# Kernel optimization log

Hardware: AMD Instinct MI355X
Metric: run time of the kernel (lower is better)

## Reference

```python
import jax, jax.numpy as jnp
import numpy as np
from jax import lax

B, S = 16, 512
H = 512          # hidden_size == embedding_dim (required by the module's own wiring)
V = 10000        # dict_len
G = 4 * H


def setup_inputs() -> dict:
    key = jax.random.key(0)
    ks = jax.random.split(key, 16)
    sc = 0.05
    inp = {
        "source": jax.random.randint(ks[0], (B, S), 0, V),
        "w_emb": jax.random.normal(ks[1], (H, V), jnp.float32) * sc,
        "b_emb": jax.random.normal(ks[2], (H,), jnp.float32) * sc,
        "w_ih0": jax.random.normal(ks[3], (G, H), jnp.float32) * sc,
        "w_hh0": jax.random.normal(ks[4], (G, H), jnp.float32) * sc,
        "b_ih0": jax.random.normal(ks[5], (G,), jnp.float32) * sc,
        "b_hh0": jax.random.normal(ks[6], (G,), jnp.float32) * sc,
        "w_ih1": jax.random.normal(ks[7], (G, H), jnp.float32) * sc,
        "w_hh1": jax.random.normal(ks[8], (G, H), jnp.float32) * sc,
        "b_ih1": jax.random.normal(ks[9], (G,), jnp.float32) * sc,
        "b_hh1": jax.random.normal(ks[10], (G,), jnp.float32) * sc,
        "w1": jax.random.normal(ks[11], (128, H), jnp.float32) * sc,
        "b1": jax.random.normal(ks[12], (128,), jnp.float32) * sc,
        "w2": jax.random.normal(ks[13], (V, 128), jnp.float32) * sc,
        "b2": jax.random.normal(ks[14], (V,), jnp.float32) * sc,
    }
    return inp


def _lstm_layer(x, w_ih, w_hh, b_ih, b_hh):
    # x: [B, S, H] -> hs: [B, S, H]; PyTorch gate order i, f, g, o
    b, s, _ = x.shape
    h_dim = w_hh.shape[1]
    # precompute input projections for all timesteps
    x_proj = jnp.einsum('bsd,gd->bsg', x, w_ih) + b_ih + b_hh  # [B, S, 4H]

    def step(carry, xt):
        h, c = carry
        gates = xt + h @ w_hh.T                      # [B, 4H]
        i, f, g, o = jnp.split(gates, 4, axis=-1)
        i = jax.nn.sigmoid(i)
        f = jax.nn.sigmoid(f)
        g = jnp.tanh(g)
        o = jax.nn.sigmoid(o)
        c = f * c + i * g
        h = o * jnp.tanh(c)
        return (h, c), h

    h0 = jnp.zeros((b, h_dim), x.dtype)
    c0 = jnp.zeros((b, h_dim), x.dtype)
    _, hs = lax.scan(step, (h0, c0), jnp.swapaxes(x_proj, 0, 1))  # [S, B, H]
    return jnp.swapaxes(hs, 0, 1)


def reference(source, w_emb, b_emb,
              w_ih0, w_hh0, b_ih0, b_hh0,
              w_ih1, w_hh1, b_ih1, b_hh1,
              w1, b1, w2, b2):
    # one_hot(source) @ w_emb.T + b_emb == row-gather of w_emb.T (identical math)
    emb = jnp.take(w_emb.T, source, axis=0) + b_emb        # [B, S, H]
    h = _lstm_layer(emb, w_ih0, w_hh0, b_ih0, b_hh0)
    h = _lstm_layer(h, w_ih1, w_hh1, b_ih1, b_hh1)         # dropout identity at eval
    hid = jax.nn.relu(jnp.einsum('bsh,kh->bsk', h, w1) + b1)  # [B, S, 128]
    logits = jnp.einsum('bsk,vk->bsv', hid, w2) + b2       # [B, S, V]
    return logits
```

## Files before the change

kernel.cpp:

```cpp
#include <hip/hip_runtime.h>
#include <hip/hip_bf16.h>

#define B_ 16
#define S_ 512
#define H_ 512
#define V_ 10000
#define G_ 2048
#define M_ (B_*S_)

typedef short bf16x8 __attribute__((ext_vector_type(8)));
typedef float f32x4 __attribute__((ext_vector_type(4)));
typedef _Float16 f16x8 __attribute__((ext_vector_type(8)));

static __device__ __forceinline__ unsigned short f2bf(float x) {
    union { float f; unsigned int u; } v; v.f = x;
    unsigned int r = v.u + 0x7fffu + ((v.u >> 16) & 1u);
    return (unsigned short)(r >> 16);
}
static __device__ __forceinline__ unsigned short f2h_bits(float x) {
    _Float16 h = (_Float16)x;
    return __builtin_bit_cast(unsigned short, h);
}
static __device__ __forceinline__ float ftanh(float x) {
    float ax = fabsf(x);
    float e  = __expf(-2.f*ax);
    float r  = (1.f - e) / (1.f + e);
    return copysignf(r, x);
}

__global__ void prep_kernel(const float* __restrict__ w_ih0, const float* __restrict__ w_hh0,
                            const float* __restrict__ b_ih0, const float* __restrict__ b_hh0,
                            const float* __restrict__ w_ih1, const float* __restrict__ w_hh1,
                            const float* __restrict__ b_ih1, const float* __restrict__ b_hh1,
                            const float* __restrict__ w1,   const float* __restrict__ w2,
                            unsigned short* __restrict__ w_ih0_b, _Float16* __restrict__ wfrag0,
                            _Float16* __restrict__ wfrag1x,      _Float16* __restrict__ wfrag1h,
                            unsigned short* __restrict__ w1_b,    unsigned short* __restrict__ w2_b,
                            float* __restrict__ bias0, float* __restrict__ bias1,
                            unsigned int* __restrict__ l1prog, unsigned int* __restrict__ lc_slot) {
    if (blockIdx.x == 0 && threadIdx.x == 0) atomicAdd(lc_slot, 1u);
    if (blockIdx.x == 0 && threadIdx.x < 64) l1prog[threadIdx.x*16] = 0u;
    int i  = blockIdx.x * blockDim.x + threadIdx.x;
    int st = gridDim.x * blockDim.x;
    for (int k = i; k < G_*H_; k += st) w_ih0_b[k] = f2bf(w_ih0[k]);
    for (int d = i; d < G_*H_; d += st) {
        int e    = d & 7;
        int l    = (d >> 3) & 63;
        int wrow = (d >> 9) & 7;
        int kc   = (d >> 12) & 15;
        int j    = (d >> 16) & 15;
        int r    = wrow*16 + (l & 15);
        int R    = (r >> 5)*512 + j*32 + (r & 31);
        int k    = kc*32 + ((l >> 4) << 3) + e;
        wfrag0[d] = (_Float16)w_hh0[R*H_ + k];
    }
    for (int d = i; d < G_*H_; d += st) {
        int e    = d & 7;
        int l    = (d >> 3) & 63;
        int nt   = (d >> 9) & 1;
        int kc   = (d >> 10) & 15;
        int j    = (d >> 14) & 63;
        int r    = nt*16 + (l & 15);
        int R    = (r >> 3)*512 + j*8 + (r & 7);
        int k    = kc*32 + ((l >> 4) << 3) + e;
        wfrag1x[d] = (_Float16)w_ih1[R*H_ + k];
        wfrag1h[d] = (_Float16)w_hh1[R*H_ + k];
    }
    for (int k = i; k < V_*128; k += st) w2_b[k] = f2bf(w2[k]);
    for (int k = i; k < 128*H_; k += st) w1_b[k] = f2bf(w1[k]);
    for (int k = i; k < G_;     k += st) { bias0[k] = b_ih0[k] + b_hh0[k]; bias1[k] = b_ih1[k] + b_hh1[k]; }
}

__global__ void embed_kernel(const int* __restrict__ src, const float* __restrict__ w_emb,
                             const float* __restrict__ b_emb, unsigned short* __restrict__ emb) {
    int m = blockIdx.x;
    int idx = src[m];
    for (int h = threadIdx.x; h < H_; h += blockDim.x)
        emb[(long)m*H_ + h] = f2bf(w_emb[(long)h*V_ + idx] + b_emb[h]);
}

template<bool RELU, bool OUT_BF16>
__launch_bounds__(256)
__global__ void gemm_kernel(const unsigned short* __restrict__ A, const unsigned short* __restrict__ Bm,
                            const float* __restrict__ bias, void* __restrict__ Cout,
                            int Ndim, int K) {
    __shared__ unsigned short At[128*40];
    __shared__ unsigned short Bt[128*40];
    int m0 = blockIdx.y * 128;
    int n0 = blockIdx.x * 128;
    int tid  = threadIdx.x;
    int lane = tid & 63, wave = tid >> 6;
    int wm = (wave >> 1) * 64, wn = (wave & 1) * 64;
    int l15 = lane & 15, l4 = lane >> 4;
    f32x4 acc[4][4] = {};

    for (int kk = 0; kk < K; kk += 32) {
        __syncthreads();
        #pragma unroll
        for (int rep = 0; rep < 2; ++rep) {
            int gid = tid + rep*256;
            int row = gid >> 2, c8 = (gid & 3) << 3;
            *(uint4*)&At[row*40 + c8] = *(const uint4*)&A[(long)(m0+row)*K + kk + c8];
            int nrow = n0 + row; if (nrow >= Ndim) nrow = Ndim - 1;
            *(uint4*)&Bt[row*40 + c8] = *(const uint4*)&Bm[(long)nrow*K + kk + c8];
        }
        __syncthreads();
        bf16x8 af[4], bfr[4];
        #pragma unroll
        for (int i = 0; i < 4; ++i)
            af[i] = *(const bf16x8*)&At[(wm + i*16 + l15)*40 + l4*8];
        #pragma unroll
        for (int j = 0; j < 4; ++j)
            bfr[j] = *(const bf16x8*)&Bt[(wn + j*16 + l15)*40 + l4*8];
        #pragma unroll
        for (int i = 0; i < 4; ++i)
            #pragma unroll
            for (int j = 0; j < 4; ++j)
                acc[i][j] = __builtin_amdgcn_mfma_f32_16x16x32_bf16(af[i], bfr[j], acc[i][j], 0, 0, 0);
    }

    #pragma unroll
    for (int i = 0; i < 4; ++i) {
        int row = m0 + wm + i*16 + l4*4;
        #pragma unroll
        for (int j = 0; j < 4; ++j) {
            int col = n0 + wn + j*16 + l15;
            if (col < Ndim) {
                float bv = bias[col];
                #pragma unroll
                for (int r = 0; r < 4; ++r) {
                    float v = acc[i][j][r] + bv;
                    if (RELU) v = v > 0.f ? v : 0.f;
                    if (OUT_BF16) ((unsigned short*)Cout)[(long)(row+r)*Ndim + col] = f2bf(v);
                    else          ((float*)Cout)[(long)(row+r)*Ndim + col] = v;
                }
            }
        }
    }
}

__launch_bounds__(512)
__global__ void lstm_fused_kernel(const float* __restrict__ xp,
                                  const uint4* __restrict__ wfrag0,
                                  const uint4* __restrict__ wfrag1x,
                                  const uint4* __restrict__ wfrag1h,
                                  const float* __restrict__ bias1,
                                  unsigned long long* __restrict__ h0ex,
                                  unsigned long long* __restrict__ h1ex,
                                  unsigned int* __restrict__ l1prog,
                                  const unsigned int* __restrict__ lc_slot,
                                  unsigned short* __restrict__ hout) {
    __shared__ __align__(16) char smem[156160];
    int tid  = threadIdx.x;
    int lane = tid & 63, wave = tid >> 6;
    int l15  = lane & 15, l4 = lane >> 4;
    unsigned int base = __hip_atomic_load(lc_slot, __ATOMIC_RELAXED, __HIP_MEMORY_SCOPE_AGENT) << 16;

    if (blockIdx.x < 16) {
        uint4*     w_lds = (uint4*)smem;
        _Float16*  h_lds = (_Float16*)(smem + 131072);
        float*     gbuf  = (float*)(smem + 131072 + 16640);
        int j = blockIdx.x;
        for (int i = tid; i < 8192; i += 512) w_lds[i] = wfrag0[(long)j*8192 + i];
        for (int i = tid; i < 4160; i += 512) ((unsigned int*)h_lds)[i] = 0;
        __syncthreads();
        const _Float16* wh = (const _Float16*)w_lds;
        int ch = tid >> 5, s = tid & 31;
        float c = 0.f;

        for (int t = 0; t < S_; ++t) {
            const float* xr = xp + ((long)ch*S_ + t)*G_ + j*32 + s;
            float xi = xr[0], xf = xr[512], xg = xr[1024], xo = xr[1536];
            if (wave == 0 && t >= 16 && (t & 7) == 0) {
                unsigned int thr = base + (unsigned int)(t - 8);
                unsigned int pv = __hip_atomic_load(l1prog + lane*16, __ATOMIC_RELAXED, __HIP_MEMORY_SCOPE_AGENT);
                while (!__all((int)(pv >= thr))) {
                    __builtin_amdgcn_s_sleep(4);
                    pv = __hip_atomic_load(l1prog + lane*16, __ATOMIC_RELAXED, __HIP_MEMORY_SCOPE_AGENT);
                }
            }
            if (t > 0) {
                unsigned int tagv = base + (unsigned int)t;
                const unsigned long long* bse = h0ex + (long)((t-1) & 15)*4096;
                unsigned long long v[8];
                for (;;) {
                    #pragma unroll
                    for (int q = 0; q < 8; ++q)
                        v[q] = __hip_atomic_load(bse + q*512 + tid, __ATOMIC_RELAXED, __HIP_MEMORY_SCOPE_AGENT);
                    bool ok = true;
                    #pragma unroll
                    for (int q = 0; q < 8; ++q)
                        ok &= ((unsigned int)(v[q] >> 32) == tagv);
                    if (ok) break;
                    __builtin_amdgcn_s_sleep(1);
                }
                #pragma unroll
                for (int q = 0; q < 8; ++q) {
                    int w = q*512 + tid;
                    *(unsigned int*)&h_lds[(w >> 8)*520 + (w & 255)*2] = (unsigned int)v[q];
                }
            }
            __syncthreads();
            f32x4 acc = {0.f,0.f,0.f,0.f};
            #pragma unroll
            for (int kc = 0; kc < 16; ++kc) {
                f16x8 af = *(const f16x8*)&h_lds[l15*520 + kc*32 + l4*8];
                f16x8 bf = *(const f16x8*)&wh[(((kc*8) + wave)*64 + lane)*8];
                acc = __builtin_amdgcn_mfma_f32_16x16x32_f16(af, bf, acc, 0, 0, 0);
            }
            #pragma unroll
            for (int r = 0; r < 4; ++r)
                gbuf[(l4*4 + r)*132 + wave*16 + l15] = acc[r];
            __syncthreads();
            const float* gb = gbuf + ch*132;
            xi += gb[s]; xf += gb[32+s]; xg += gb[64+s]; xo += gb[96+s];
            float ig = 1.f/(1.f+__expf(-xi));
            float fg = 1.f/(1.f+__expf(-xf));
            float gg = ftanh(xg);
            float og = 1.f/(1.f+__expf(-xo));
            c = fg*c + ig*gg;
            float h = og*ftanh(c);
            unsigned int me = f2h_bits(h);
            unsigned int up = (unsigned int)__shfl_down((int)me, 1, 64);
            if (!(s & 1)) {
                unsigned long long vv = ((unsigned long long)(base + (unsigned int)(t+1)) << 32)
                                      | (up << 16) | me;
                __hip_atomic_store(&h0ex[(long)(t & 15)*4096 + ch*256 + j*16 + (s>>1)], vv,
                                   __ATOMIC_RELAXED, __HIP_MEMORY_SCOPE_AGENT);
            }
        }
    } else {
        uint4*     wx   = (uint4*)smem;
        uint4*     whh  = wx + 2048;
        _Float16*  h0l  = (_Float16*)(smem + 65536);
        _Float16*  h1l  = h0l + 16*520;
        float*     gbuf = (float*)(smem + 65536 + 2*16640);
        float*     bl   = gbuf + 2*2*16*36;
        int j1 = blockIdx.x - 16;
        for (int i = tid; i < 2048; i += 512) {
            wx[i]  = wfrag1x[(long)j1*2048 + i];
            whh[i] = wfrag1h[(long)j1*2048 + i];
        }
        if (tid < 32) bl[tid] = bias1[(tid >> 3)*512 + j1*8 + (tid & 7)];
        for (int i = tid; i < 8320; i += 512) ((unsigned int*)h0l)[i] = 0;
        __syncthreads();
        int ch = tid >> 3, sc = tid & 7;
        float c = 0.f;

        for (int t = 0; t < S_; ++t) {
            {
                unsigned int tag0 = base + (unsigned int)(t+1);
                unsigned int tag1 = base + (unsigned int)t;
                const unsigned long long* b0 = h0ex + (long)(t & 15)*4096;
                const unsigned long long* b1 = h1ex + (long)((t > 0 ? t-1 : 0) & 3)*4096;
                unsigned long long v0[8], v1[8];
                for (;;) {
                    #pragma unroll
                    for (int q = 0; q < 8; ++q)
                        v0[q] = __hip_atomic_load(b0 + q*512 + tid, __ATOMIC_RELAXED, __HIP_MEMORY_SCOPE_AGENT);
                    if (t > 0) {
                        #pragma unroll
                        for (int q = 0; q < 8; ++q)
                            v1[q] = __hip_atomic_load(b1 + q*512 + tid, __ATOMIC_RELAXED, __HIP_MEMORY_SCOPE_AGENT);
                    }
                    bool ok = true;
                    #pragma unroll
                    for (int q = 0; q < 8; ++q)
                        ok &= ((unsigned int)(v0[q] >> 32) == tag0);
                    if (t > 0) {
                        #pragma unroll
                        for (int q = 0; q < 8; ++q)
                            ok &= ((unsigned int)(v1[q] >> 32) == tag1);
                    }
                    if (ok) break;
                    __builtin_amdgcn_s_sleep(1);
                }
                if (t > 0) {
                    #pragma unroll
                    for (int q = 0; q < 8; ++q) {
                        int w = q*512 + tid;
                        *(unsigned int*)&h1l[(w >> 8)*520 + (w & 255)*2] = (unsigned int)v1[q];
                    }
                }
                #pragma unroll
                for (int q = 0; q < 8; ++q) {
                    int w = q*512 + tid;
                    *(unsigned int*)&h0l[(w >> 8)*520 + (w & 255)*2] = (unsigned int)v0[q];
                }
            }
            __syncthreads();
            if (tid == 0)
                __hip_atomic_store(l1prog + j1*16, base + (unsigned int)t,
                                   __ATOMIC_RELAXED, __HIP_MEMORY_SCOPE_AGENT);
            {
                int src = wave >> 2, nt = (wave >> 1) & 1, kh = wave & 1;
                const _Float16* hs = src ? h1l : h0l;
                const _Float16* ws = (const _Float16*)(src ? whh : wx);
                f32x4 acc = {0.f,0.f,0.f,0.f};
                #pragma unroll
                for (int k2 = 0; k2 < 8; ++k2) {
                    int kc = kh*8 + k2;
                    f16x8 af = *(const f16x8*)&hs[l15*520 + kc*32 + l4*8];
                    f16x8 bf = *(const f16x8*)&ws[((kc*2 + nt)*64 + lane)*8];
                    acc = __builtin_amdgcn_mfma_f32_16x16x32_f16(af, bf, acc, 0, 0, 0);
                }
                #pragma unroll
                for (int r = 0; r < 4; ++r)
                    gbuf[((src*2 + kh)*16 + (l4*4 + r))*36 + nt*16 + l15] = acc[r];
            }
            __syncthreads();
            if (tid < 128) {
                const float* g0 = gbuf + (0*16 + ch)*36;
                const float* g1 = gbuf + (1*16 + ch)*36;
                const float* g2 = gbuf + (2*16 + ch)*36;
                const float* g3 = gbuf + (3*16 + ch)*36;
                float xi = g0[sc]    + g1[sc]    + g2[sc]    + g3[sc]    + bl[sc];
                float xf = g0[8+sc]  + g1[8+sc]  + g2[8+sc]  + g3[8+sc]  + bl[8+sc];
                float xg = g0[16+sc] + g1[16+sc] + g2[16+sc] + g3[16+sc] + bl[16+sc];
                float xo = g0[24+sc] + g1[24+sc] + g2[24+sc] + g3[24+sc] + bl[24+sc];
                float ig = 1.f/(1.f+__expf(-xi));
                float fg = 1.f/(1.f+__expf(-xf));
                float gg = ftanh(xg);
                float og = 1.f/(1.f+__expf(-xo));
                c = fg*c + ig*gg;
                float h = og*ftanh(c);
                hout[((long)ch*S_ + t)*H_ + j1*8 + sc] = f2bf(h);
                unsigned int me = f2h_bits(h);
                unsigned int up = (unsigned int)__shfl_down((int)me, 1, 64);
                if (!(sc & 1)) {
                    unsigned long long vv = ((unsigned long long)(base + (unsigned int)(t+1)) << 32)
                                          | (up << 16) | me;
                    __hip_atomic_store(&h1ex[(long)(t & 3)*4096 + ch*256 + j1*4 + (sc>>1)], vv,
                                       __ATOMIC_RELAXED, __HIP_MEMORY_SCOPE_AGENT);
                }
            }
        }
    }
}

extern "C" void kernel_launch(void* const* d_in, const int* in_sizes, int n_in,
                              void* d_out, int out_size, void* d_ws, size_t ws_size,
                              hipStream_t stream) {
    const int*   src   = (const int*)  d_in[0];
    const float* w_emb = (const float*)d_in[1];
    const float* b_emb = (const float*)d_in[2];
    const float* w_ih0 = (const float*)d_in[3];
    const float* w_hh0 = (const float*)d_in[4];
    const float* b_ih0 = (const float*)d_in[5];
    const float* b_hh0 = (const float*)d_in[6];
    const float* w_ih1 = (const float*)d_in[7];
    const float* w_hh1 = (const float*)d_in[8];
    const float* b_ih1 = (const float*)d_in[9];
    const float* b_hh1 = (const float*)d_in[10];
    const float* w1    = (const float*)d_in[11];
    const float* b1    = (const float*)d_in[12];
    const float* w2    = (const float*)d_in[13];
    const float* b2    = (const float*)d_in[14];
    float* out = (float*)d_out;

    char* ws = (char*)d_ws;
    size_t off = 0;
    auto alloc = [&](size_t bytes) -> void* {
        void* p = ws + off;
        off = (off + bytes + 255) & ~(size_t)255;
        return p;
    };
    unsigned short* w_ih0_b = (unsigned short*)alloc((size_t)G_*H_*2);
    _Float16*       wfrag0  = (_Float16*)      alloc((size_t)G_*H_*2);
    _Float16*       wfrag1x = (_Float16*)      alloc((size_t)G_*H_*2);
    _Float16*       wfrag1h = (_Float16*)      alloc((size_t)G_*H_*2);
    unsigned short* w1_b    = (unsigned short*)alloc((size_t)128*H_*2);
    unsigned short* w2_b    = (unsigned short*)alloc((size_t)V_*128*2);
    float*          bias0   = (float*)         alloc((size_t)G_*4);
    float*          bias1   = (float*)         alloc((size_t)G_*4);
    unsigned short* emb     = (unsigned short*)alloc((size_t)M_*H_*2);
    unsigned short* hidb    = (unsigned short*)alloc((size_t)M_*128*2);
    float*          xp      = (float*)         alloc((size_t)M_*G_*4);
    unsigned long long* h0ex = (unsigned long long*)alloc((size_t)16*4096*8);
    unsigned long long* h1ex = (unsigned long long*)alloc((size_t)4*4096*8);
    unsigned int*   l1prog  = (unsigned int*)  alloc((size_t)64*16*4);
    unsigned int*   lc_slot = (unsigned int*)  alloc((size_t)256);

    prep_kernel<<<2048, 256, 0, stream>>>(w_ih0, w_hh0, b_ih0, b_hh0,
                                          w_ih1, w_hh1, b_ih1, b_hh1,
                                          w1, w2,
                                          w_ih0_b, wfrag0, wfrag1x, wfrag1h,
                                          w1_b, w2_b, bias0, bias1,
                                          l1prog, lc_slot);
    embed_kernel<<<M_, 256, 0, stream>>>(src, w_emb, b_emb, emb);

    gemm_kernel<false,false><<<dim3(G_/128, M_/128), 256, 0, stream>>>(emb, w_ih0_b, bias0, xp, G_, H_);

    lstm_fused_kernel<<<80, 512, 0, stream>>>(xp, (const uint4*)wfrag0,
                                              (const uint4*)wfrag1x, (const uint4*)wfrag1h,
                                              bias1, h0ex, h1ex, l1prog, lc_slot, emb);

    gemm_kernel<true,true><<<dim3(1, M_/128), 256, 0, stream>>>(emb, w1_b, b1, hidb, 128, H_);

    gemm_kernel<false,false><<<dim3((V_+127)/128, M_/128), 256, 0, stream>>>(hidb, w2_b, b2, out, V_, 128);
}
```

Before: 2.458 ms.

## Place LSTM blocks on one XCD, mirror h exchange via local-cache loads

Launches 256 blocks and keeps only those with bid%8 equal to 0 or 1, so the 16 layer-0 blocks and 32 layer-1 blocks are presumably co-located on the same XCD under round-robin dispatch. The hidden-state exchange is mirrored into a buffer written and read with sc0 loads and stores, which may hit a shared cache faster than device-scope atomics, with a fallback to the coherent path after repeated misses. Recurrent weights move from LDS into registers, layer 1 is repartitioned into 16-column slices with 32 blocks, and the layer-1 wait is split so h0 loads are issued before polling h1. This relies on the dispatch placement assumption and sc0 coherence semantics, and it raises register pressure.

```diff
diff --git a/kernel.cpp b/kernel.cpp
--- a/kernel.cpp
+++ b/kernel.cpp
@@ -11,6 +11,7 @@
 typedef short bf16x8 __attribute__((ext_vector_type(8)));
 typedef float f32x4 __attribute__((ext_vector_type(4)));
 typedef _Float16 f16x8 __attribute__((ext_vector_type(8)));
+typedef unsigned int u32x4 __attribute__((ext_vector_type(4)));
 
 static __device__ __forceinline__ unsigned short f2bf(float x) {
     union { float f; unsigned int u; } v; v.f = x;
@@ -26,6 +27,19 @@
     float e  = __expf(-2.f*ax);
     float r  = (1.f - e) / (1.f + e);
     return copysignf(r, x);
+}
+
+static __device__ __forceinline__ void ld64_sc0(const void* p, u32x4& a, u32x4& b, u32x4& c, u32x4& d) {
+    asm volatile("global_load_dwordx4 %0, %4, off sc0\n\t"
+                 "global_load_dwordx4 %1, %4, off offset:16 sc0\n\t"
+                 "global_load_dwordx4 %2, %4, off offset:32 sc0\n\t"
+                 "global_load_dwordx4 %3, %4, off offset:48 sc0\n\t"
+                 "s_waitcnt vmcnt(0)"
+                 : "=&v"(a), "=&v"(b), "=&v"(c), "=&v"(d)
+                 : "v"(p) : "memory");
+}
+static __device__ __forceinline__ void st_sc0(void* p, unsigned long long v) {
+    asm volatile("global_store_dwordx2 %0, %1, off sc0" :: "v"(p), "v"(v) : "memory");
 }
 
 __global__ void prep_kernel(const float* __restrict__ w_ih0, const float* __restrict__ w_hh0,
@@ -55,14 +69,13 @@
         wfrag0[d] = (_Float16)w_hh0[R*H_ + k];
     }
     for (int d = i; d < G_*H_; d += st) {
-        int e    = d & 7;
-        int l    = (d >> 3) & 63;
-        int nt   = (d >> 9) & 1;
-        int kc   = (d >> 10) & 15;
-        int j    = (d >> 14) & 63;
-        int r    = nt*16 + (l & 15);
-        int R    = (r >> 3)*512 + j*8 + (r & 7);
-        int k    = kc*32 + ((l >> 4) << 3) + e;
+        int e  = d & 7;
+        int l  = (d >> 3) & 63;
+        int nt = (d >> 9) & 3;
+        int kc = (d >> 11) & 15;
+        int j  = (d >> 15) & 31;
+        int R  = nt*512 + j*16 + (l & 15);
+        int k  = kc*32 + ((l >> 4) << 3) + e;
         wfrag1x[d] = (_Float16)w_ih1[R*H_ + k];
         wfrag1h[d] = (_Float16)w_hh1[R*H_ + k];
     }
@@ -141,72 +154,99 @@
 
 __launch_bounds__(512)
 __global__ void lstm_fused_kernel(const float* __restrict__ xp,
-                                  const uint4* __restrict__ wfrag0,
-                                  const uint4* __restrict__ wfrag1x,
-                                  const uint4* __restrict__ wfrag1h,
+                                  const _Float16* __restrict__ wfrag0,
+                                  const _Float16* __restrict__ wfrag1x,
+                                  const _Float16* __restrict__ wfrag1h,
                                   const float* __restrict__ bias1,
                                   unsigned long long* __restrict__ h0ex,
                                   unsigned long long* __restrict__ h1ex,
+                                  unsigned long long* __restrict__ h0mir,
+                                  unsigned long long* __restrict__ h1mir,
                                   unsigned int* __restrict__ l1prog,
                                   const unsigned int* __restrict__ lc_slot,
                                   unsigned short* __restrict__ hout) {
-    __shared__ __align__(16) char smem[156160];
+    __shared__ __align__(16) char smem[98304];
+    int bid = blockIdx.x;
+    int mod = bid & 7, grp = bid >> 3;
+    bool isL0 = (mod == 0) && (grp < 16);
+    bool isL1 = (mod == 1) && (grp < 32);
+    if (!isL0 && !isL1) return;
+
     int tid  = threadIdx.x;
     int lane = tid & 63, wave = tid >> 6;
     int l15  = lane & 15, l4 = lane >> 4;
     unsigned int base = __hip_atomic_load(lc_slot, __ATOMIC_RELAXED, __HIP_MEMORY_SCOPE_AGENT) << 16;
 
-    if (blockIdx.x < 16) {
-        uint4*     w_lds = (uint4*)smem;
-        _Float16*  h_lds = (_Float16*)(smem + 131072);
-        float*     gbuf  = (float*)(smem + 131072 + 16640);
-        int j = blockIdx.x;
-        for (int i = tid; i < 8192; i += 512) w_lds[i] = wfrag0[(long)j*8192 + i];
-        for (int i = tid; i < 4160; i += 512) ((unsigned int*)h_lds)[i] = 0;
+    if (isL0) {
+        _Float16* h_lds = (_Float16*)smem;
+        float*    gbuf  = (float*)(smem + 16640);
+        int j = grp;
+        const f16x8* w0g = (const f16x8*)wfrag0 + (long)j*8192;
+        f16x8 bfr[16];
+        #pragma unroll
+        for (int kc = 0; kc < 16; ++kc) bfr[kc] = w0g[(kc*8 + wave)*64 + lane];
+        for (int i2 = tid; i2 < 4160; i2 += 512) ((unsigned int*)h_lds)[i2] = 0;
         __syncthreads();
-        const _Float16* wh = (const _Float16*)w_lds;
         int ch = tid >> 5, s = tid & 31;
         float c = 0.f;
+        bool useLocal = true; int miss = 0;
 
         for (int t = 0; t < S_; ++t) {
             const float* xr = xp + ((long)ch*S_ + t)*G_ + j*32 + s;
             float xi = xr[0], xf = xr[512], xg = xr[1024], xo = xr[1536];
             if (wave == 0 && t >= 16 && (t & 7) == 0) {
                 unsigned int thr = base + (unsigned int)(t - 8);
-                unsigned int pv = __hip_atomic_load(l1prog + lane*16, __ATOMIC_RELAXED, __HIP_MEMORY_SCOPE_AGENT);
+                unsigned int pv = __hip_atomic_load(l1prog + (lane & 31)*16, __ATOMIC_RELAXED, __HIP_MEMORY_SCOPE_AGENT);
                 while (!__all((int)(pv >= thr))) {
                     __builtin_amdgcn_s_sleep(4);
-                    pv = __hip_atomic_load(l1prog + lane*16, __ATOMIC_RELAXED, __HIP_MEMORY_SCOPE_AGENT);
+                    pv = __hip_atomic_load(l1prog + (lane & 31)*16, __ATOMIC_RELAXED, __HIP_MEMORY_SCOPE_AGENT);
                 }
             }
             if (t > 0) {
                 unsigned int tagv = base + (unsigned int)t;
-                const unsigned long long* bse = h0ex + (long)((t-1) & 15)*4096;
-                unsigned long long v[8];
-                for (;;) {
-                    #pragma unroll
-                    for (int q = 0; q < 8; ++q)
-                        v[q] = __hip_atomic_load(bse + q*512 + tid, __ATOMIC_RELAXED, __HIP_MEMORY_SCOPE_AGENT);
-                    bool ok = true;
-                    #pragma unroll
-                    for (int q = 0; q < 8; ++q)
-                        ok &= ((unsigned int)(v[q] >> 32) == tagv);
-                    if (ok) break;
-                    __builtin_amdgcn_s_sleep(1);
-                }
-                #pragma unroll
-                for (int q = 0; q < 8; ++q) {
-                    int w = q*512 + tid;
-                    *(unsigned int*)&h_lds[(w >> 8)*520 + (w & 255)*2] = (unsigned int)v[q];
-                }
+                long slab = (long)((t-1) & 15) * 4096;
+                u32x4 pa, pb, pc, pd;
+                bool got = false;
+                if (useLocal) {
+                    const unsigned long long* mb = h0mir + slab + (long)tid*8;
+                    for (int r = 0; r < 16; ++r) {
+                        ld64_sc0(mb, pa, pb, pc, pd);
+                        if (pa.y==tagv && pa.w==tagv && pb.y==tagv && pb.w==tagv &&
+                            pc.y==tagv && pc.w==tagv && pd.y==tagv && pd.w==tagv) { got = true; break; }
+                        __builtin_amdgcn_s_sleep(1);
+                    }
+                }
+                if (!got) {
+                    const unsigned long long* gb8 = h0ex + slab + (long)tid*8;
+                    unsigned long long v[8];
+                    int ar = 0;
+                    for (;;) {
+                        #pragma unroll
+                        for (int q = 0; q < 8; ++q)
+                            v[q] = __hip_atomic_load(gb8 + q, __ATOMIC_RELAXED, __HIP_MEMORY_SCOPE_AGENT);
+                        bool ok = true;
+                        #pragma unroll
+                        for (int q = 0; q < 8; ++q) ok &= ((unsigned int)(v[q] >> 32) == tagv);
+                        if (ok) break;
+                        ++ar;
+                        __builtin_amdgcn_s_sleep(1);
+                    }
+                    if (useLocal && ar == 0 && ++miss >= 4) useLocal = false;
+                    pa.x=(unsigned int)v[0]; pa.z=(unsigned int)v[1];
+                    pb.x=(unsigned int)v[2]; pb.z=(unsigned int)v[3];
+                    pc.x=(unsigned int)v[4]; pc.z=(unsigned int)v[5];
+                    pd.x=(unsigned int)v[6]; pd.z=(unsigned int)v[7];
+                }
+                unsigned int* hl = (unsigned int*)&h_lds[ch*520 + s*16];
+                hl[0]=pa.x; hl[1]=pa.z; hl[2]=pb.x; hl[3]=pb.z;
+                hl[4]=pc.x; hl[5]=pc.z; hl[6]=pd.x; hl[7]=pd.z;
             }
             __syncthreads();
             f32x4 acc = {0.f,0.f,0.f,0.f};
             #pragma unroll
             for (int kc = 0; kc < 16; ++kc) {
                 f16x8 af = *(const f16x8*)&h_lds[l15*520 + kc*32 + l4*8];
-                f16x8 bf = *(const f16x8*)&wh[(((kc*8) + wave)*64 + lane)*8];
-                acc = __builtin_amdgcn_mfma_f32_16x16x32_f16(af, bf, acc, 0, 0, 0);
+                acc = __builtin_amdgcn_mfma_f32_16x16x32_f16(af, bfr[kc], acc, 0, 0, 0);
             }
             #pragma unroll
             for (int r = 0; r < 4; ++r)
@@ -225,61 +265,89 @@
             if (!(s & 1)) {
                 unsigned long long vv = ((unsigned long long)(base + (unsigned int)(t+1)) << 32)
                                       | (up << 16) | me;
-                __hip_atomic_store(&h0ex[(long)(t & 15)*4096 + ch*256 + j*16 + (s>>1)], vv,
-                                   __ATOMIC_RELAXED, __HIP_MEMORY_SCOPE_AGENT);
+                long slot = (long)(t & 15)*4096 + ch*256 + j*16 + (s>>1);
+                __hip_atomic_store(&h0ex[slot], vv, __ATOMIC_RELAXED, __HIP_MEMORY_SCOPE_AGENT);
+                st_sc0((void*)&h0mir[slot], vv);
             }
         }
     } else {
-        uint4*     wx   = (uint4*)smem;
-        uint4*     whh  = wx + 2048;
-        _Float16*  h0l  = (_Float16*)(smem + 65536);
-        _Float16*  h1l  = h0l + 16*520;
-        float*     gbuf = (float*)(smem + 65536 + 2*16640);
-        float*     bl   = gbuf + 2*2*16*36;
-        int j1 = blockIdx.x - 16;
-        for (int i = tid; i < 2048; i += 512) {
-            wx[i]  = wfrag1x[(long)j1*2048 + i];
-            whh[i] = wfrag1h[(long)j1*2048 + i];
-        }
-        if (tid < 32) bl[tid] = bias1[(tid >> 3)*512 + j1*8 + (tid & 7)];
-        for (int i = tid; i < 8320; i += 512) ((unsigned int*)h0l)[i] = 0;
+        _Float16* h0l  = (_Float16*)smem;
+        _Float16* h1l  = h0l + 16*520;
+        float*    gbuf = (float*)(smem + 33280);
+        float*    bl   = (float*)(smem + 33280 + 8704);
+        int j1 = grp;
+        int ntw = wave & 3, srcw = wave >> 2;
+        const f16x8* wsrc = ((const f16x8*)(srcw ? wfrag1h : wfrag1x)) + (long)j1*4096;
+        f16x8 bfr[16];
+        #pragma unroll
+        for (int kc = 0; kc < 16; ++kc) bfr[kc] = wsrc[(kc*4 + ntw)*64 + lane];
+        if (tid < 64) bl[tid] = bias1[(tid >> 4)*512 + j1*16 + (tid & 15)];
+        for (int i2 = tid; i2 < 8320; i2 += 512) ((unsigned int*)h0l)[i2] = 0;
         __syncthreads();
-        int ch = tid >> 3, sc = tid & 7;
+        int ch = tid >> 4, sc = tid & 15;
         float c = 0.f;
+        bool useLocal = true; int miss = 0;
 
         for (int t = 0; t < S_; ++t) {
+            unsigned int tag0 = base + (unsigned int)(t+1);
+            unsigned int tag1 = base + (unsigned int)t;
+            const unsigned long long* b0 = h0ex + (long)(t & 15)*4096;
+            unsigned long long v0[8];
+            #pragma unroll
+            for (int q = 0; q < 8; ++q)
+                v0[q] = __hip_atomic_load(b0 + q*512 + tid, __ATOMIC_RELAXED, __HIP_MEMORY_SCOPE_AGENT);
+            if (t > 0) {
+                long slab1 = (long)((t-1) & 3)*4096;
+                u32x4 pa, pb, pc, pd;
+                bool got = false;
+                if (useLocal) {
+                    const unsigned long long* mb = h1mir + slab1 + (long)tid*8;
+                    for (int r = 0; r < 16; ++r) {
+                        ld64_sc0(mb, pa, pb, pc, pd);
+                        if (pa.y==tag1 && pa.w==tag1 && pb.y==tag1 && pb.w==tag1 &&
+                            pc.y==tag1 && pc.w==tag1 && pd.y==tag1 && pd.w==tag1) { got = true; break; }
+                        __builtin_amdgcn_s_sleep(1);
+                    }
+                }
+                if (!got) {
+                    const unsigned long long* gb8 = h1ex + slab1 + (long)tid*8;
+                    unsigned long long v[8];
+                    int ar = 0;
+                    for (;;) {
+                        #pragma unroll
+                        for (int q = 0; q < 8; ++q)
+                            v[q] = __hip_atomic_load(gb8 + q, __ATOMIC_RELAXED, __HIP_MEMORY_SCOPE_AGENT);
+                        bool ok = true;
+                        #pragma unroll
+                        for (int q = 0; q < 8; ++q) ok &= ((unsigned int)(v[q] >> 32) == tag1);
+                        if (ok) break;
+                        ++ar;
+                        __builtin_amdgcn_s_sleep(1);
+                    }
+                    if (useLocal && ar == 0 && ++miss >= 4) useLocal = false;
+                    pa.x=(unsigned int)v[0]; pa.z=(unsigned int)v[1];
+                    pb.x=(unsigned int)v[2]; pb.z=(unsigned int)v[3];
+                    pc.x=(unsigned int)v[4]; pc.z=(unsigned int)v[5];
+                    pd.x=(unsigned int)v[6]; pd.z=(unsigned int)v[7];
+                }
+                unsigned int* hl = (unsigned int*)&h1l[(tid >> 5)*520 + (tid & 31)*16];
+                hl[0]=pa.x; hl[1]=pa.z; hl[2]=pb.x; hl[3]=pb.z;
+                hl[4]=pc.x; hl[5]=pc.z; hl[6]=pd.x; hl[7]=pd.z;
+            }
             {
-                unsigned int tag0 = base + (unsigned int)(t+1);
-                unsigned int tag1 = base + (unsigned int)t;
-                const unsigned long long* b0 = h0ex + (long)(t & 15)*4096;
-                const unsigned long long* b1 = h1ex + (long)((t > 0 ? t-1 : 0) & 3)*4096;
-                unsigned long long v0[8], v1[8];
-                for (;;) {
-                    #pragma unroll
-                    for (int q = 0; q < 8; ++q)
-                        v0[q] = __hip_atomic_load(b0 + q*512 + tid, __ATOMIC_RELAXED, __HIP_MEMORY_SCOPE_AGENT);
-                    if (t > 0) {
+                bool ok0 = true;
+                #pragma unroll
+                for (int q = 0; q < 8; ++q) ok0 &= ((unsigned int)(v0[q] >> 32) == tag0);
+                if (!ok0) {
+                    for (;;) {
                         #pragma unroll
                         for (int q = 0; q < 8; ++q)
-                            v1[q] = __hip_atomic_load(b1 + q*512 + tid, __ATOMIC_RELAXED, __HIP_MEMORY_SCOPE_AGENT);
-                    }
-                    bool ok = true;
-                    #pragma unroll
-                    for (int q = 0; q < 8; ++q)
-                        ok &= ((unsigned int)(v0[q] >> 32) == tag0);
-                    if (t > 0) {
-                        #pragma unroll
-                        for (int q = 0; q < 8; ++q)
-                            ok &= ((unsigned int)(v1[q] >> 32) == tag1);
-                    }
-                    if (ok) break;
-                    __builtin_amdgcn_s_sleep(1);
-                }
-                if (t > 0) {
-                    #pragma unroll
-                    for (int q = 0; q < 8; ++q) {
-                        int w = q*512 + tid;
-                        *(unsigned int*)&h1l[(w >> 8)*520 + (w & 255)*2] = (unsigned int)v1[q];
+                            v0[q] = __hip_atomic_load(b0 + q*512 + tid, __ATOMIC_RELAXED, __HIP_MEMORY_SCOPE_AGENT);
+                        bool ok = true;
+                        #pragma unroll
+                        for (int q = 0; q < 8; ++q) ok &= ((unsigned int)(v0[q] >> 32) == tag0);
+                        if (ok) break;
+                        __builtin_amdgcn_s_sleep(1);
                     }
                 }
                 #pragma unroll
@@ -293,45 +361,38 @@
                 __hip_atomic_store(l1prog + j1*16, base + (unsigned int)t,
                                    __ATOMIC_RELAXED, __HIP_MEMORY_SCOPE_AGENT);
             {
-                int src = wave >> 2, nt = (wave >> 1) & 1, kh = wave & 1;
-                const _Float16* hs = src ? h1l : h0l;
-                const _Float16* ws = (const _Float16*)(src ? whh : wx);
+                const _Float16* hs = srcw ? h1l : h0l;
                 f32x4 acc = {0.f,0.f,0.f,0.f};
                 #pragma unroll
-                for (int k2 = 0; k2 < 8; ++k2) {
-                    int kc = kh*8 + k2;
+                for (int kc = 0; kc < 16; ++kc) {
                     f16x8 af = *(const f16x8*)&hs[l15*520 + kc*32 + l4*8];
-                    f16x8 bf = *(const f16x8*)&ws[((kc*2 + nt)*64 + lane)*8];
-                    acc = __builtin_amdgcn_mfma_f32_16x16x32_f16(af, bf, acc, 0, 0, 0);
+                    acc = __builtin_amdgcn_mfma_f32_16x16x32_f16(af, bfr[kc], acc, 0, 0, 0);
                 }
                 #pragma unroll
                 for (int r = 0; r < 4; ++r)
-                    gbuf[((src*2 + kh)*16 + (l4*4 + r))*36 + nt*16 + l15] = acc[r];
+                    gbuf[(wave*16 + l4*4 + r)*17 + l15] = acc[r];
             }
             __syncthreads();
-            if (tid < 128) {
-                const float* g0 = gbuf + (0*16 + ch)*36;
-                const float* g1 = gbuf + (1*16 + ch)*36;
-                const float* g2 = gbuf + (2*16 + ch)*36;
-                const float* g3 = gbuf + (3*16 + ch)*36;
-                float xi = g0[sc]    + g1[sc]    + g2[sc]    + g3[sc]    + bl[sc];
-                float xf = g0[8+sc]  + g1[8+sc]  + g2[8+sc]  + g3[8+sc]  + bl[8+sc];
-                float xg = g0[16+sc] + g1[16+sc] + g2[16+sc] + g3[16+sc] + bl[16+sc];
-                float xo = g0[24+sc] + g1[24+sc] + g2[24+sc] + g3[24+sc] + bl[24+sc];
+            if (tid < 256) {
+                float xi = gbuf[((0*4+0)*16+ch)*17+sc] + gbuf[((1*4+0)*16+ch)*17+sc] + bl[sc];
+                float xf = gbuf[((0*4+1)*16+ch)*17+sc] + gbuf[((1*4+1)*16+ch)*17+sc] + bl[16+sc];
+                float xg = gbuf[((0*4+2)*16+ch)*17+sc] + gbuf[((1*4+2)*16+ch)*17+sc] + bl[32+sc];
+                float xo = gbuf[((0*4+3)*16+ch)*17+sc] + gbuf[((1*4+3)*16+ch)*17+sc] + bl[48+sc];
                 float ig = 1.f/(1.f+__expf(-xi));
                 float fg = 1.f/(1.f+__expf(-xf));
                 float gg = ftanh(xg);
                 float og = 1.f/(1.f+__expf(-xo));
                 c = fg*c + ig*gg;
                 float h = og*ftanh(c);
-                hout[((long)ch*S_ + t)*H_ + j1*8 + sc] = f2bf(h);
+                hout[((long)ch*S_ + t)*H_ + j1*16 + sc] = f2bf(h);
                 unsigned int me = f2h_bits(h);
                 unsigned int up = (unsigned int)__shfl_down((int)me, 1, 64);
                 if (!(sc & 1)) {
                     unsigned long long vv = ((unsigned long long)(base + (unsigned int)(t+1)) << 32)
                                           | (up << 16) | me;
-                    __hip_atomic_store(&h1ex[(long)(t & 3)*4096 + ch*256 + j1*4 + (sc>>1)], vv,
-                                       __ATOMIC_RELAXED, __HIP_MEMORY_SCOPE_AGENT);
+                    long slot = (long)(t & 3)*4096 + ch*256 + j1*8 + (sc>>1);
+                    __hip_atomic_store(&h1ex[slot], vv, __ATOMIC_RELAXED, __HIP_MEMORY_SCOPE_AGENT);
+                    st_sc0((void*)&h1mir[slot], vv);
                 }
             }
         }
@@ -376,8 +437,10 @@
     unsigned short* emb     = (unsigned short*)alloc((size_t)M_*H_*2);
     unsigned short* hidb    = (unsigned short*)alloc((size_t)M_*128*2);
     float*          xp      = (float*)         alloc((size_t)M_*G_*4);
-    unsigned long long* h0ex = (unsigned long long*)alloc((size_t)16*4096*8);
-    unsigned long long* h1ex = (unsigned long long*)alloc((size_t)4*4096*8);
+    unsigned long long* h0ex  = (unsigned long long*)alloc((size_t)16*4096*8);
+    unsigned long long* h1ex  = (unsigned long long*)alloc((size_t)4*4096*8);
+    unsigned long long* h0mir = (unsigned long long*)alloc((size_t)16*4096*8);
+    unsigned long long* h1mir = (unsigned long long*)alloc((size_t)4*4096*8);
     unsigned int*   l1prog  = (unsigned int*)  alloc((size_t)64*16*4);
     unsigned int*   lc_slot = (unsigned int*)  alloc((size_t)256);
 
@@ -391,9 +454,9 @@
 
     gemm_kernel<false,false><<<dim3(G_/128, M_/128), 256, 0, stream>>>(emb, w_ih0_b, bias0, xp, G_, H_);
 
-    lstm_fused_kernel<<<80, 512, 0, stream>>>(xp, (const uint4*)wfrag0,
-                                              (const uint4*)wfrag1x, (const uint4*)wfrag1h,
-                                              bias1, h0ex, h1ex, l1prog, lc_slot, emb);
+    lstm_fused_kernel<<<256, 512, 0, stream>>>(xp, wfrag0, wfrag1x, wfrag1h,
+                                               bias1, h0ex, h1ex, h0mir, h1mir,
+                                               l1prog, lc_slot, emb);
 
     gemm_kernel<true,true><<<dim3(1, M_/128), 256, 0, stream>>>(emb, w1_b, b1, hidb, 128, H_);
 
```

Measured after the change: 2.654 ms. 1.08x slower.
